# Optimization experiments

Measured on AMD Instinct MI355X. Metric: run time of the kernel, lower is better.

The kernel has to match this reference:

```python
import jax, jax.numpy as jnp
import numpy as np

MIN_NORM = 1e-15
BALL_EPS = 4e-3  # HGCN PoincareBall fp32 boundary eps
C = 1.0          # curvature (init kwarg c)
CLAMP = 1e6      # torch.clamp bound in HypAgg.forward


def _artanh(x):
    # torch Artanh clamps input into open (-1, 1); use fp32-safe eps
    return jnp.arctanh(jnp.clip(x, -1.0 + 1e-7, 1.0 - 1e-7))


def _norm(x):
    return jnp.maximum(jnp.linalg.norm(x, axis=-1, keepdims=True), MIN_NORM)


def mobius_add(x, y, c):
    x2 = jnp.sum(x * x, axis=-1, keepdims=True)
    y2 = jnp.sum(y * y, axis=-1, keepdims=True)
    xy = jnp.sum(x * y, axis=-1, keepdims=True)
    num = (1.0 + 2.0 * c * xy + c * y2) * x + (1.0 - c * x2) * y
    den = 1.0 + 2.0 * c * xy + (c * c) * x2 * y2
    return num / jnp.maximum(den, MIN_NORM)


def lambda_x(x, c):
    return 2.0 / jnp.maximum(1.0 - c * jnp.sum(x * x, axis=-1, keepdims=True), MIN_NORM)


def logmap(p1, p2, c):
    # log_{p1}(p2) on the Poincare ball
    sub = mobius_add(-p1, p2, c)
    sub_norm = _norm(sub)
    sqrt_c = c ** 0.5
    return (2.0 / sqrt_c / lambda_x(p1, c)) * _artanh(sqrt_c * sub_norm) * sub / sub_norm


def expmap(u, p, c):
    sqrt_c = c ** 0.5
    u_norm = _norm(u)
    second = jnp.tanh(sqrt_c / 2.0 * lambda_x(p, c) * u_norm) * u / (sqrt_c * u_norm)
    return mobius_add(p, second, c)


def proj(x, c):
    norm = _norm(x)
    maxnorm = (1.0 - BALL_EPS) / (c ** 0.5)
    return jnp.where(norm > maxnorm, x / norm * maxnorm, x)


def setup_inputs() -> dict:
    key = jax.random.key(0)
    kx, ka, kw = jax.random.split(key, 3)
    B, N, D = 2, 768, 64
    # points strictly inside the unit ball
    x = proj(0.2 * jax.random.normal(kx, (B, N, D), dtype=jnp.float32), C)
    adj = (jax.random.uniform(ka, (B, N, N), dtype=jnp.float32) < 0.05).astype(jnp.float32)
    att_W = jax.random.normal(kw, (2 * D, 1), dtype=jnp.float32) * (1.0 / np.sqrt(2 * D))
    att_b = jnp.zeros((1,), dtype=jnp.float32)
    return {"x": x, "adj": adj, "att_W": att_W, "att_b": att_b}


def reference(x, adj, att_W, att_b):
    c = C
    b, n, d = x.shape
    # pairwise tangent vectors: x_local[b,i,j] = log_{x_i}(x_j)   (b,n,n,d)
    x_i = x[:, :, None, :]
    x_j = x[:, None, :, :]
    x_local = logmap(x_i, x_j, c)
    # log_x(x) == 0 tangent, kept for faithfulness
    x_self = logmap(x, x, c)  # (b,n,d), ~0
    # DenseAtt: linear(2d->1) on [self_tangent || pairwise_tangent], sigmoid, masked by adj
    feats = jnp.concatenate(
        [jnp.broadcast_to(x_self[:, :, None, :], x_local.shape), x_local], axis=-1
    )  # (b,n,n,2d)
    logits = jnp.einsum('bijk,ko->bijo', feats, att_W)[..., 0] + att_b[0]  # (b,n,n)
    att = jax.nn.sigmoid(logits) * adj
    # attention-weighted tangent aggregation over neighbors j
    support_t = jnp.einsum('bij,bijd->bid', att, x_local)
    # proj_tan is identity on the Poincare ball
    support_t = jnp.clip(support_t, -CLAMP, CLAMP)
    return proj(expmap(support_t, x, c), c)
```

## Files before the change

kernel.cpp:

```cpp
#include <hip/hip_runtime.h>
#include <math.h>

#define NB 2
#define NN 768
#define ND 64
#define XSTRIDE 68

__device__ __forceinline__ float fmul_(float a, float b) { float r = a * b; asm volatile("" : "+v"(r)); return r; }
__device__ __forceinline__ float fadd_(float a, float b) { float r = a + b; asm volatile("" : "+v"(r)); return r; }

template <typename F>
__device__ __forceinline__ float pw64(F f) {
  float r[8];
#pragma unroll
  for (int m = 0; m < 8; ++m) r[m] = f(m);
#pragma unroll
  for (int i = 1; i < 8; ++i) {
#pragma unroll
    for (int m = 0; m < 8; ++m) r[m] = fadd_(r[m], f(8 * i + m));
  }
  const float s01 = fadd_(r[0], r[1]), s23 = fadd_(r[2], r[3]);
  const float s45 = fadd_(r[4], r[5]), s67 = fadd_(r[6], r[7]);
  return fadd_(fadd_(s01, s23), fadd_(s45, s67));
}

__device__ __forceinline__ float pwShfl(float v, int lane) {
  const int m = lane & 7;
  float s = __shfl(v, m);
#pragma unroll
  for (int i = 1; i < 8; ++i) s = fadd_(s, __shfl(v, m + 8 * i));
  s = fadd_(s, __shfl_xor(s, 1));
  s = fadd_(s, __shfl_xor(s, 2));
  s = fadd_(s, __shfl_xor(s, 4));
  return s;
}

__device__ __forceinline__ void pwShfl2(float va, float vb, int lane,
                                        float& sa, float& sb) {
  const int m = lane & 7;
  float a = __shfl(va, m), b = __shfl(vb, m);
#pragma unroll
  for (int i = 1; i < 8; ++i) {
    a = fadd_(a, __shfl(va, m + 8 * i));
    b = fadd_(b, __shfl(vb, m + 8 * i));
  }
  a = fadd_(a, __shfl_xor(a, 1)); b = fadd_(b, __shfl_xor(b, 1));
  a = fadd_(a, __shfl_xor(a, 2)); b = fadd_(b, __shfl_xor(b, 2));
  a = fadd_(a, __shfl_xor(a, 4)); b = fadd_(b, __shfl_xor(b, 4));
  sa = a; sb = b;
}

__device__ __forceinline__ float div_rn(float n, float d, float r) {
  const float q0 = n * r;
  const float e  = __builtin_fmaf(-d, q0, n);
  return __builtin_fmaf(e, r, q0);
}

__global__ __launch_bounds__(64) void k_main(const float* __restrict__ x,
                                             const float* __restrict__ adj,
                                             const float* __restrict__ attW,
                                             const float* __restrict__ attb,
                                             float* __restrict__ out) {
  __shared__ float xi_s[ND];
  __shared__ float sW2[ND];
  __shared__ short lj[NN];
  __shared__ float lds_x[64 * XSTRIDE];

  const int row  = blockIdx.x;
  const int b    = row / NN;
  const int lane = threadIdx.x;

  const float xiv = x[(size_t)row * ND + lane];
  xi_s[lane] = xiv;
  sW2[lane]  = attW[ND + lane];

  const float* __restrict__ arow = adj + (size_t)row * NN;
  float av[NN / 64];
#pragma unroll
  for (int c = 0; c < NN / 64; ++c) av[c] = arow[c * 64 + lane];

  const float ni = pwShfl(fmul_(xiv, xiv), lane);

  const float b1  = 1.0f - ni;
  const float lam = 2.0f / fmaxf(b1, 1e-15f);
  const float g1  = 2.0f / lam;
  const float ab  = attb[0];
  const float ATH_CLIP = (float)(1.0 - 1e-07);

  int count = 0, qb1 = 0, qb2 = 0, qb3 = 0;
#pragma unroll
  for (int c = 0; c < NN / 64; ++c) {
    const unsigned long long m = __ballot(av[c] != 0.0f);
    if (av[c] != 0.0f) {
      const int rank = __popcll(m & ((1ull << lane) - 1ull));
      lj[count + rank] = (short)(c * 64 + lane);
    }
    count += __popcll(m);
    if (c == 2) qb1 = count;
    if (c == 5) qb2 = count;
    if (c == 8) qb3 = count;
  }
  __syncthreads();

  const float* __restrict__ xb = x + (size_t)b * NN * ND;
  float pP = 0.0f;
  float Q0 = 0.0f, Q1 = 0.0f, Q2 = 0.0f, Q3 = 0.0f;
  float cfv = 0.0f;

  for (int base = 0; base < count; base += 64) {
    const int valid = min(count - base, 64);

    if (lane < valid) {
      const int j = lj[base + lane];
      float rj[ND];
      const float4* __restrict__ xj4 = (const float4*)(xb + (size_t)j * ND);
#pragma unroll
      for (int k4 = 0; k4 < 16; ++k4) {
        const float4 v = xj4[k4];
        rj[4 * k4 + 0] = v.x; rj[4 * k4 + 1] = v.y;
        rj[4 * k4 + 2] = v.z; rj[4 * k4 + 3] = v.w;
      }
      {
        float4* __restrict__ dst = (float4*)&lds_x[lane * XSTRIDE];
#pragma unroll
        for (int k4 = 0; k4 < 16; ++k4)
          dst[k4] = make_float4(rj[4 * k4], rj[4 * k4 + 1],
                                rj[4 * k4 + 2], rj[4 * k4 + 3]);
      }
      const float nj = pw64([&](int k) { return fmul_(rj[k], rj[k]); });
      const float d  = pw64([&](int k) { return fmul_(xi_s[k], rj[k]); });
      const float xy = -d;
      const float t1  = fadd_(1.0f, 2.0f * xy);
      const float a1  = fadd_(t1, nj);
      const float den = fadd_(t1, fmul_(ni, nj));
      const float denc = fmaxf(den, 1e-15f);
      const float rden = 1.0f / denc;
      float racc[8];
      float subW = 0.0f;
#pragma unroll
      for (int m = 0; m < 8; ++m) {
        const float nk = fadd_(-fmul_(a1, xi_s[m]), fmul_(b1, rj[m]));
        const float sk = div_rn(nk, denc, rden);
        subW = __builtin_fmaf(sk, sW2[m], subW);
        racc[m] = fmul_(sk, sk);
      }
#pragma unroll
      for (int i8 = 1; i8 < 8; ++i8) {
#pragma unroll
        for (int m = 0; m < 8; ++m) {
          const int k = 8 * i8 + m;
          const float nk = fadd_(-fmul_(a1, xi_s[k]), fmul_(b1, rj[k]));
          const float sk = div_rn(nk, denc, rden);
          subW = __builtin_fmaf(sk, sW2[k], subW);
          racc[m] = fadd_(racc[m], fmul_(sk, sk));
        }
      }
      const float s01 = fadd_(racc[0], racc[1]), s23 = fadd_(racc[2], racc[3]);
      const float s45 = fadd_(racc[4], racc[5]), s67 = fadd_(racc[6], racc[7]);
      const float s2  = fadd_(fadd_(s01, s23), fadd_(s45, s67));
      const float t   = sqrtf(s2);
      const float sn  = fmaxf(t, 1e-15f);
      const float z   = fminf(sn, ATH_CLIP);
      const float ath = atanhf(z);
      const float g2  = fmul_(g1, ath);
      const float gg  = g2 / sn;
      const float logit = gg * subW + ab;
      const float sig   = 1.0f / (1.0f + expf(-logit));
      const float cfac  = sig * gg * rden;
      cfv = cfac;
      pP = __builtin_fmaf(cfac, a1, pP);
    }
    __syncthreads();

    const int lim = base + valid;
    {
      const int lo = max(0,   base), hi = min(qb1, lim);
      for (int p2 = lo; p2 < hi; ++p2)
        Q0 = __builtin_fmaf(__shfl(cfv, p2 - base),
                            lds_x[(p2 - base) * XSTRIDE + lane], Q0);
    }
    {
      const int lo = max(qb1, base), hi = min(qb2, lim);
      for (int p2 = lo; p2 < hi; ++p2)
        Q1 = __builtin_fmaf(__shfl(cfv, p2 - base),
                            lds_x[(p2 - base) * XSTRIDE + lane], Q1);
    }
    {
      const int lo = max(qb2, base), hi = min(qb3, lim);
      for (int p2 = lo; p2 < hi; ++p2)
        Q2 = __builtin_fmaf(__shfl(cfv, p2 - base),
                            lds_x[(p2 - base) * XSTRIDE + lane], Q2);
    }
    {
      const int lo = max(qb3, base), hi = min(count, lim);
      for (int p2 = lo; p2 < hi; ++p2)
        Q3 = __builtin_fmaf(__shfl(cfv, p2 - base),
                            lds_x[(p2 - base) * XSTRIDE + lane], Q3);
    }
    __syncthreads();
  }

  float pw = pP;
#pragma unroll
  for (int m = 32; m >= 1; m >>= 1) pw += __shfl_xor(pw, m, 64);
  const float P = pw;
  const float Q = (Q0 + Q1) + (Q2 + Q3);

  float u = b1 * Q - P * xiv;
  u = fminf(fmaxf(u, -1e6f), 1e6f);
  const float u2 = pwShfl(fmul_(u, u), lane);
  const float un = fmaxf(sqrtf(u2), 1e-15f);
  const float th = tanhf(fmul_(0.5f * lam, un));
  const float sec = fmul_(th, u) / un;
  float y2, xys;
  pwShfl2(fmul_(sec, sec), fmul_(xiv, sec), lane, y2, xys);
  const float t1e  = fadd_(1.0f, 2.0f * xys);
  const float a1e  = fadd_(t1e, y2);
  const float dene = fmaxf(fadd_(t1e, fmul_(ni, y2)), 1e-15f);
  const float o    = fadd_(fmul_(a1e, xiv), fmul_(b1, sec)) / dene;
  const float o2 = pwShfl(fmul_(o, o), lane);
  const float nm = fmaxf(sqrtf(o2), 1e-15f);
  const float res = (nm > 0.996f) ? fmul_(o / nm, 0.996f) : o;
  out[(size_t)row * ND + lane] = res;
}

extern "C" void kernel_launch(void* const* d_in, const int* in_sizes, int n_in,
                              void* d_out, int out_size, void* d_ws, size_t ws_size,
                              hipStream_t stream) {
  const float* x    = (const float*)d_in[0];
  const float* adj  = (const float*)d_in[1];
  const float* attW = (const float*)d_in[2];
  const float* attb = (const float*)d_in[3];
  float* out = (float*)d_out;

  hipLaunchKernelGGL(k_main, dim3(NB * NN), dim3(64), 0, stream,
                     x, adj, attW, attb, out);
}
```

Measured before the change: 74.18 us.

## Software-pipeline neighbor aggregation via LDS coefficients and use butterfly reductions

Per-neighbor coefficients now go through shared memory instead of being broadcast with __shfl, and the Q accumulation loop prefetches four entries ahead to hide LDS latency. The mid-loop __syncthreads is dropped, which works only because the block is a single wavefront. The dot product with the attention weights is split into eight partial accumulators to shorten its dependency chain. The epilogue replaces the shuffle-gather reductions with full xor butterflies, which changes the floating-point summation order and may differ slightly from the earlier results.

New measurement: 74.89 us. Within noise of the previous version (+1.0%).

```diff
diff --git a/kernel.cpp b/kernel.cpp
--- a/kernel.cpp
+++ b/kernel.cpp
@@ -35,19 +35,14 @@
   return s;
 }
 
-__device__ __forceinline__ void pwShfl2(float va, float vb, int lane,
-                                        float& sa, float& sb) {
-  const int m = lane & 7;
-  float a = __shfl(va, m), b = __shfl(vb, m);
-#pragma unroll
-  for (int i = 1; i < 8; ++i) {
-    a = fadd_(a, __shfl(va, m + 8 * i));
-    b = fadd_(b, __shfl(vb, m + 8 * i));
-  }
-  a = fadd_(a, __shfl_xor(a, 1)); b = fadd_(b, __shfl_xor(b, 1));
-  a = fadd_(a, __shfl_xor(a, 2)); b = fadd_(b, __shfl_xor(b, 2));
-  a = fadd_(a, __shfl_xor(a, 4)); b = fadd_(b, __shfl_xor(b, 4));
-  sa = a; sb = b;
+__device__ __forceinline__ float bfly(float v) {
+  v = fadd_(v, __shfl_xor(v, 1));
+  v = fadd_(v, __shfl_xor(v, 2));
+  v = fadd_(v, __shfl_xor(v, 4));
+  v = fadd_(v, __shfl_xor(v, 8));
+  v = fadd_(v, __shfl_xor(v, 16));
+  v = fadd_(v, __shfl_xor(v, 32));
+  return v;
 }
 
 __device__ __forceinline__ float div_rn(float n, float d, float r) {
@@ -64,6 +59,7 @@
   __shared__ float xi_s[ND];
   __shared__ float sW2[ND];
   __shared__ short lj[NN];
+  __shared__ float cf_s[64];
   __shared__ float lds_x[64 * XSTRIDE];
 
   const int row  = blockIdx.x;
@@ -105,7 +101,6 @@
   const float* __restrict__ xb = x + (size_t)b * NN * ND;
   float pP = 0.0f;
   float Q0 = 0.0f, Q1 = 0.0f, Q2 = 0.0f, Q3 = 0.0f;
-  float cfv = 0.0f;
 
   for (int base = 0; base < count; base += 64) {
     const int valid = min(count - base, 64);
@@ -136,12 +131,12 @@
       const float denc = fmaxf(den, 1e-15f);
       const float rden = 1.0f / denc;
       float racc[8];
-      float subW = 0.0f;
+      float sw[8];
 #pragma unroll
       for (int m = 0; m < 8; ++m) {
         const float nk = fadd_(-fmul_(a1, xi_s[m]), fmul_(b1, rj[m]));
         const float sk = div_rn(nk, denc, rden);
-        subW = __builtin_fmaf(sk, sW2[m], subW);
+        sw[m]   = __builtin_fmaf(sk, sW2[m], 0.0f);
         racc[m] = fmul_(sk, sk);
       }
 #pragma unroll
@@ -151,13 +146,16 @@
           const int k = 8 * i8 + m;
           const float nk = fadd_(-fmul_(a1, xi_s[k]), fmul_(b1, rj[k]));
           const float sk = div_rn(nk, denc, rden);
-          subW = __builtin_fmaf(sk, sW2[k], subW);
+          sw[m]   = __builtin_fmaf(sk, sW2[k], sw[m]);
           racc[m] = fadd_(racc[m], fmul_(sk, sk));
         }
       }
       const float s01 = fadd_(racc[0], racc[1]), s23 = fadd_(racc[2], racc[3]);
       const float s45 = fadd_(racc[4], racc[5]), s67 = fadd_(racc[6], racc[7]);
       const float s2  = fadd_(fadd_(s01, s23), fadd_(s45, s67));
+      const float w01 = fadd_(sw[0], sw[1]), w23 = fadd_(sw[2], sw[3]);
+      const float w45 = fadd_(sw[4], sw[5]), w67 = fadd_(sw[6], sw[7]);
+      const float subW = fadd_(fadd_(w01, w23), fadd_(w45, w67));
       const float t   = sqrtf(s2);
       const float sn  = fmaxf(t, 1e-15f);
       const float z   = fminf(sn, ATH_CLIP);
@@ -167,36 +165,35 @@
       const float logit = gg * subW + ab;
       const float sig   = 1.0f / (1.0f + expf(-logit));
       const float cfac  = sig * gg * rden;
-      cfv = cfac;
+      cf_s[lane] = cfac;
       pP = __builtin_fmaf(cfac, a1, pP);
     }
-    __syncthreads();
 
     const int lim = base + valid;
-    {
-      const int lo = max(0,   base), hi = min(qb1, lim);
-      for (int p2 = lo; p2 < hi; ++p2)
-        Q0 = __builtin_fmaf(__shfl(cfv, p2 - base),
-                            lds_x[(p2 - base) * XSTRIDE + lane], Q0);
-    }
-    {
-      const int lo = max(qb1, base), hi = min(qb2, lim);
-      for (int p2 = lo; p2 < hi; ++p2)
-        Q1 = __builtin_fmaf(__shfl(cfv, p2 - base),
-                            lds_x[(p2 - base) * XSTRIDE + lane], Q1);
-    }
-    {
-      const int lo = max(qb2, base), hi = min(qb3, lim);
-      for (int p2 = lo; p2 < hi; ++p2)
-        Q2 = __builtin_fmaf(__shfl(cfv, p2 - base),
-                            lds_x[(p2 - base) * XSTRIDE + lane], Q2);
-    }
-    {
-      const int lo = max(qb3, base), hi = min(count, lim);
-      for (int p2 = lo; p2 < hi; ++p2)
-        Q3 = __builtin_fmaf(__shfl(cfv, p2 - base),
-                            lds_x[(p2 - base) * XSTRIDE + lane], Q3);
-    }
+    auto qloop = [&](int lo, int hi, float& Q) {
+      if (lo >= hi) return;
+      const int last = hi - 1 - base;
+      const int i0 = lo - base;
+      const int i1 = min(i0 + 1, last);
+      const int i2 = min(i0 + 2, last);
+      const int i3 = min(i0 + 3, last);
+      float c0 = cf_s[i0], v0 = lds_x[i0 * XSTRIDE + lane];
+      float c1 = cf_s[i1], v1 = lds_x[i1 * XSTRIDE + lane];
+      float c2 = cf_s[i2], v2 = lds_x[i2 * XSTRIDE + lane];
+      float c3 = cf_s[i3], v3 = lds_x[i3 * XSTRIDE + lane];
+#pragma unroll 4
+      for (int p = lo; p < hi; ++p) {
+        const int in = min(p - base + 4, last);
+        const float cn = cf_s[in];
+        const float vn = lds_x[in * XSTRIDE + lane];
+        Q = __builtin_fmaf(c0, v0, Q);
+        c0 = c1; v0 = v1; c1 = c2; v1 = v2; c2 = c3; v2 = v3; c3 = cn; v3 = vn;
+      }
+    };
+    qloop(base,           min(qb1, lim),   Q0);
+    qloop(max(qb1, base), min(qb2, lim),   Q1);
+    qloop(max(qb2, base), min(qb3, lim),   Q2);
+    qloop(max(qb3, base), min(count, lim), Q3);
     __syncthreads();
   }
 
@@ -208,17 +205,17 @@
 
   float u = b1 * Q - P * xiv;
   u = fminf(fmaxf(u, -1e6f), 1e6f);
-  const float u2 = pwShfl(fmul_(u, u), lane);
+  const float u2 = bfly(fmul_(u, u));
   const float un = fmaxf(sqrtf(u2), 1e-15f);
   const float th = tanhf(fmul_(0.5f * lam, un));
   const float sec = fmul_(th, u) / un;
-  float y2, xys;
-  pwShfl2(fmul_(sec, sec), fmul_(xiv, sec), lane, y2, xys);
+  const float y2  = bfly(fmul_(sec, sec));
+  const float xys = bfly(fmul_(xiv, sec));
   const float t1e  = fadd_(1.0f, 2.0f * xys);
   const float a1e  = fadd_(t1e, y2);
   const float dene = fmaxf(fadd_(t1e, fmul_(ni, y2)), 1e-15f);
   const float o    = fadd_(fmul_(a1e, xiv), fmul_(b1, sec)) / dene;
-  const float o2 = pwShfl(fmul_(o, o), lane);
+  const float o2 = bfly(fmul_(o, o));
   const float nm = fmaxf(sqrtf(o2), 1e-15f);
   const float res = (nm > 0.996f) ? fmul_(o / nm, 0.996f) : o;
   out[(size_t)row * ND + lane] = res;
```
